# Kernel optimization log

Measured on AMD Instinct MI355X. Metric: run time of the kernel, lower is better.

Reference implementation:

```python
import jax, jax.numpy as jnp
import numpy as np

THRESH_FACTOR = 0.7  # standard TTQ threshold: 0.7 * mean(|W|)

def ternary_quantize(w):
    delta = THRESH_FACTOR * jnp.mean(jnp.abs(w))
    # {-1, 0, +1} ternary weights
    return jnp.where(w > delta, 1.0, jnp.where(w < -delta, -1.0, 0.0)).astype(w.dtype)

def setup_inputs() -> dict:
    key = jax.random.key(0)
    k1, k2, k3 = jax.random.split(key, 3)
    B, S, D_IN, D_OUT = 8, 4096, 1024, 1024
    inp = {
        "input": jax.random.normal(k1, (B, S, D_IN), dtype=jnp.float32),
        "weight": jax.random.normal(k2, (D_OUT, D_IN), dtype=jnp.float32) * (1.0 / np.sqrt(D_IN)),
        "alpha": jnp.ones((1,), dtype=jnp.float32),
        "bias": jax.random.normal(k3, (D_OUT,), dtype=jnp.float32) * (1.0 / np.sqrt(D_IN)),
    }
    return inp

def reference(input, weight, alpha, bias):
    w_ternary = ternary_quantize(weight)          # [out, in] in {-1,0,1}
    w_eff = w_ternary * alpha                     # scalar alpha scale
    # F.linear: y = x @ W^T + b
    out = jnp.einsum('bsd,od->bso', input, w_eff) + bias
    return out
```

## Files before the change

kernel.cpp:

```cpp
#include <hip/hip_runtime.h>
#include <hip/hip_bf16.h>

typedef __bf16 bf16;
typedef __attribute__((ext_vector_type(8))) __bf16 bf16x8;
typedef __attribute__((ext_vector_type(4))) __bf16 bf16x4;
typedef __attribute__((ext_vector_type(4))) float f32x4;

__device__ __forceinline__ void async_load16(const void* g, void* l) {
    __builtin_amdgcn_global_load_lds(
        (const __attribute__((address_space(1))) void*)g,
        (__attribute__((address_space(3))) void*)l, 16, 0, 0);
}

__global__ __launch_bounds__(256) void k_abs_part(const float* __restrict__ w, int n,
                                                  double* __restrict__ part) {
    __shared__ double sd[256];
    const int per_block = n / gridDim.x;
    const int base = blockIdx.x * per_block;
    double s = 0.0;
    for (int i = threadIdx.x; i < per_block; i += 256)
        s += (double)fabsf(w[base + i]);
    sd[threadIdx.x] = s;
    __syncthreads();
    for (int off = 128; off > 0; off >>= 1) {
        if (threadIdx.x < off) sd[threadIdx.x] += sd[threadIdx.x + off];
        __syncthreads();
    }
    if (threadIdx.x == 0) part[blockIdx.x] = sd[0];
}

__global__ __launch_bounds__(256) void k_delta(const double* __restrict__ part, int npart,
                                               int n, float* __restrict__ delta) {
    __shared__ double sd[256];
    double s = 0.0;
    for (int i = threadIdx.x; i < npart; i += 256) s += part[i];
    sd[threadIdx.x] = s;
    __syncthreads();
    for (int off = 128; off > 0; off >>= 1) {
        if (threadIdx.x < off) sd[threadIdx.x] += sd[threadIdx.x + off];
        __syncthreads();
    }
    if (threadIdx.x == 0) *delta = (float)(0.7 * sd[0] / (double)n);
}

__global__ __launch_bounds__(256) void k_quant(const float* __restrict__ w,
                                               const float* __restrict__ dp,
                                               bf16* __restrict__ wt, int n4) {
    const float d = *dp;
    const int i = blockIdx.x * 256 + threadIdx.x;
    if (i >= n4) return;
    const float4 v = ((const float4*)w)[i];
    bf16x4 o;
    o[0] = (bf16)((v.x > d) ? 1.0f : (v.x < -d) ? -1.0f : 0.0f);
    o[1] = (bf16)((v.y > d) ? 1.0f : (v.y < -d) ? -1.0f : 0.0f);
    o[2] = (bf16)((v.z > d) ? 1.0f : (v.z < -d) ? -1.0f : 0.0f);
    o[3] = (bf16)((v.w > d) ? 1.0f : (v.w < -d) ? -1.0f : 0.0f);
    *(bf16x4*)(wt + (size_t)i * 4) = o;
}

__global__ __launch_bounds__(256) void k_gemm(const float* __restrict__ A,
                                              const bf16* __restrict__ Bw,
                                              const float* __restrict__ alphap,
                                              const float* __restrict__ bias,
                                              float* __restrict__ C,
                                              int M, int N, int K) {
    __shared__ bf16 As[128 * 32];
    __shared__ bf16 Bs[128 * 32];

    const int t    = threadIdx.x;
    const int lane = t & 63;
    const int wave = t >> 6;
    const int nbm  = M >> 7;
    const int bm0  = (blockIdx.x % nbm) << 7;
    const int bn0  = (blockIdx.x / nbm) << 7;
    const int wr   = (wave >> 1) << 6;
    const int wc   = (wave & 1) << 6;

    f32x4 acc[4][4] = {};

    const int lr = lane & 15;
    const int lk = (lane >> 4) << 3;

    for (int k0 = 0; k0 < K; k0 += 32) {
        #pragma unroll
        for (int j = 0; j < 2; ++j) {
            const int c = t + j * 256;
            const bf16* src = Bw + (size_t)(bn0 + (c >> 2)) * K + k0 + ((c & 3) << 3);
            async_load16(src, (char*)Bs + j * 4096 + wave * 1024);
        }
        #pragma unroll
        for (int i = 0; i < 4; ++i) {
            const int idx = t + i * 256;
            const int row = idx >> 3;
            const int c4  = (idx & 7) << 2;
            const float4 v = *(const float4*)(A + (size_t)(bm0 + row) * K + k0 + c4);
            bf16x4 h;
            h[0] = (bf16)v.x; h[1] = (bf16)v.y; h[2] = (bf16)v.z; h[3] = (bf16)v.w;
            *(bf16x4*)(As + row * 32 + c4) = h;
        }
        __syncthreads();

        bf16x8 af[4], bfr[4];
        #pragma unroll
        for (int m = 0; m < 4; ++m)
            af[m] = *(const bf16x8*)(As + (wr + m * 16 + lr) * 32 + lk);
        #pragma unroll
        for (int n = 0; n < 4; ++n)
            bfr[n] = *(const bf16x8*)(Bs + (wc + n * 16 + lr) * 32 + lk);
        #pragma unroll
        for (int m = 0; m < 4; ++m)
            #pragma unroll
            for (int n = 0; n < 4; ++n)
                acc[m][n] = __builtin_amdgcn_mfma_f32_16x16x32_bf16(af[m], bfr[n], acc[m][n], 0, 0, 0);
        __syncthreads();
    }

    const float alpha = *alphap;
    float bv[4];
    #pragma unroll
    for (int n = 0; n < 4; ++n) bv[n] = bias[bn0 + wc + n * 16 + lr];

    #pragma unroll
    for (int m = 0; m < 4; ++m) {
        #pragma unroll
        for (int n = 0; n < 4; ++n) {
            const int gcol = bn0 + wc + n * 16 + lr;
            #pragma unroll
            for (int r = 0; r < 4; ++r) {
                const int grow = bm0 + wr + m * 16 + ((lane >> 4) << 2) + r;
                C[(size_t)grow * N + gcol] = alpha * acc[m][n][r] + bv[n];
            }
        }
    }
}

extern "C" void kernel_launch(void* const* d_in, const int* in_sizes, int n_in,
                              void* d_out, int out_size, void* d_ws, size_t ws_size,
                              hipStream_t stream) {
    const float* x     = (const float*)d_in[0];
    const float* w     = (const float*)d_in[1];
    const float* alpha = (const float*)d_in[2];
    const float* bias  = (const float*)d_in[3];
    float* out = (float*)d_out;

    const int wn   = in_sizes[1];
    const int dout = in_sizes[3];
    const int din  = wn / dout;
    const int m    = in_sizes[0] / din;

    char* ws = (char*)d_ws;
    float*  delta = (float*)ws;
    double* part  = (double*)(ws + 64);
    bf16*   wt    = (bf16*)(ws + 8192);

    k_abs_part<<<256, 256, 0, stream>>>(w, wn, part);
    k_delta<<<1, 256, 0, stream>>>(part, 256, wn, delta);
    k_quant<<<(wn / 4 + 255) / 256, 256, 0, stream>>>(w, delta, wt, wn / 4);

    dim3 grid((m / 128) * (dout / 128));
    k_gemm<<<grid, 256, 0, stream>>>(x, wt, alpha, bias, out, m, dout, din);
}
```

Measured before the change: 140.5 us.

## Double-buffer GEMM tiles with BK=64, XOR-swizzled LDS, and XCD-aware block mapping

Rewrites the GEMM main loop to double-buffer the A and B tiles in LDS with a K-tile of 64. The next tile's global loads are issued before the current tile's MFMAs, and the converted A values are written to LDS afterwards, so memory latency overlaps compute and one barrier per iteration is removed. LDS rows are XOR-swizzled in 16-byte slots to avoid bank conflicts, and block IDs are remapped across the 8 XCDs so that N-adjacent tiles sharing A rows land on the same XCD. The cost is doubled LDS (64 KB per block) and more registers for the prefetched floats, with launch_bounds(256,2) set to keep two blocks per CU.

```diff
diff --git a/kernel.cpp b/kernel.cpp
--- a/kernel.cpp
+++ b/kernel.cpp
@@ -58,76 +58,134 @@
     *(bf16x4*)(wt + (size_t)i * 4) = o;
 }
 
-__global__ __launch_bounds__(256) void k_gemm(const float* __restrict__ A,
-                                              const bf16* __restrict__ Bw,
-                                              const float* __restrict__ alphap,
-                                              const float* __restrict__ bias,
-                                              float* __restrict__ C,
-                                              int M, int N, int K) {
-    __shared__ bf16 As[128 * 32];
-    __shared__ bf16 Bs[128 * 32];
+__global__ __launch_bounds__(256, 2) void k_gemm(const float* __restrict__ A,
+                                                 const bf16* __restrict__ Bw,
+                                                 const float* __restrict__ alphap,
+                                                 const float* __restrict__ bias,
+                                                 float* __restrict__ C,
+                                                 int M, int N, int K) {
+    __shared__ __align__(16) bf16 As[2][128 * 64];
+    __shared__ __align__(16) bf16 Bs[2][128 * 64];
 
     const int t    = threadIdx.x;
     const int lane = t & 63;
     const int wave = t >> 6;
-    const int nbm  = M >> 7;
-    const int bm0  = (blockIdx.x % nbm) << 7;
-    const int bn0  = (blockIdx.x / nbm) << 7;
-    const int wr   = (wave >> 1) << 6;
-    const int wc   = (wave & 1) << 6;
+
+    const int nbn = N >> 7;
+    const int cpx = gridDim.x >> 3;
+    const int lid = (blockIdx.x & 7) * cpx + (blockIdx.x >> 3);
+    const int bn0 = (lid & (nbn - 1)) << 7;
+    const int bm0 = (lid / nbn) << 7;
+
+    const int wr = (wave >> 1) << 6;
+    const int wc = (wave & 1) << 6;
+    const int lr = lane & 15;
+    const int hi = lane >> 4;
 
     f32x4 acc[4][4] = {};
 
-    const int lr = lane & 15;
-    const int lk = (lane >> 4) << 3;
-
-    for (int k0 = 0; k0 < K; k0 += 32) {
-        #pragma unroll
-        for (int j = 0; j < 2; ++j) {
-            const int c = t + j * 256;
-            const bf16* src = Bw + (size_t)(bn0 + (c >> 2)) * K + k0 + ((c & 3) << 3);
-            async_load16(src, (char*)Bs + j * 4096 + wave * 1024);
-        }
-        #pragma unroll
-        for (int i = 0; i < 4; ++i) {
-            const int idx = t + i * 256;
-            const int row = idx >> 3;
-            const int c4  = (idx & 7) << 2;
-            const float4 v = *(const float4*)(A + (size_t)(bm0 + row) * K + k0 + c4);
-            bf16x4 h;
-            h[0] = (bf16)v.x; h[1] = (bf16)v.y; h[2] = (bf16)v.z; h[3] = (bf16)v.w;
-            *(bf16x4*)(As + row * 32 + c4) = h;
-        }
-        __syncthreads();
-
-        bf16x8 af[4], bfr[4];
-        #pragma unroll
-        for (int m = 0; m < 4; ++m)
-            af[m] = *(const bf16x8*)(As + (wr + m * 16 + lr) * 32 + lk);
-        #pragma unroll
-        for (int n = 0; n < 4; ++n)
-            bfr[n] = *(const bf16x8*)(Bs + (wc + n * 16 + lr) * 32 + lk);
-        #pragma unroll
-        for (int m = 0; m < 4; ++m)
-            #pragma unroll
-            for (int n = 0; n < 4; ++n)
-                acc[m][n] = __builtin_amdgcn_mfma_f32_16x16x32_bf16(af[m], bfr[n], acc[m][n], 0, 0, 0);
-        __syncthreads();
+    const int a_slot = t & 7;
+    const int a_row0 = t >> 3;
+    const int b_cl   = (wave << 6) | lane;
+    const int b_row0 = b_cl >> 3;
+    const int b_slot = lane & 7;
+
+    const int NT = K >> 6;
+    int cur = 0;
+
+    {
+        #pragma unroll
+        for (int j = 0; j < 4; ++j) {
+            const int row = (j << 5) + b_row0;
+            const int ss  = b_slot ^ (row & 7);
+            async_load16(Bw + (size_t)(bn0 + row) * K + (ss << 3),
+                         (char*)&Bs[0][0] + (j << 12) + (wave << 10));
+        }
+        #pragma unroll
+        for (int u = 0; u < 4; ++u) {
+            const int row = (u << 5) + a_row0;
+            const float4 v0 = *(const float4*)(A + (size_t)(bm0 + row) * K + (a_slot << 3));
+            const float4 v1 = *(const float4*)(A + (size_t)(bm0 + row) * K + (a_slot << 3) + 4);
+            bf16x8 h;
+            h[0] = (bf16)v0.x; h[1] = (bf16)v0.y; h[2] = (bf16)v0.z; h[3] = (bf16)v0.w;
+            h[4] = (bf16)v1.x; h[5] = (bf16)v1.y; h[6] = (bf16)v1.z; h[7] = (bf16)v1.w;
+            *(bf16x8*)((char*)&As[0][0] + row * 128 + ((a_slot ^ (row & 7)) << 4)) = h;
+        }
+        __syncthreads();
+    }
+
+    for (int kt = 0; kt < NT; ++kt) {
+        const int nxt = cur ^ 1;
+        const bool pf = (kt + 1) < NT;
+        const int kn = (kt + 1) << 6;
+        float4 av[8];
+
+        if (pf) {
+            #pragma unroll
+            for (int j = 0; j < 4; ++j) {
+                const int row = (j << 5) + b_row0;
+                const int ss  = b_slot ^ (row & 7);
+                async_load16(Bw + (size_t)(bn0 + row) * K + kn + (ss << 3),
+                             (char*)&Bs[nxt][0] + (j << 12) + (wave << 10));
+            }
+            #pragma unroll
+            for (int u = 0; u < 4; ++u) {
+                const int row = (u << 5) + a_row0;
+                av[2 * u]     = *(const float4*)(A + (size_t)(bm0 + row) * K + kn + (a_slot << 3));
+                av[2 * u + 1] = *(const float4*)(A + (size_t)(bm0 + row) * K + kn + (a_slot << 3) + 4);
+            }
+        }
+
+        #pragma unroll
+        for (int ksub = 0; ksub < 2; ++ksub) {
+            const int ls = (ksub << 2) + hi;
+            bf16x8 af[4], bfm[4];
+            #pragma unroll
+            for (int m = 0; m < 4; ++m) {
+                const int row = wr + (m << 4) + lr;
+                af[m] = *(const bf16x8*)((char*)&As[cur][0] + row * 128 + ((ls ^ (row & 7)) << 4));
+            }
+            #pragma unroll
+            for (int n = 0; n < 4; ++n) {
+                const int row = wc + (n << 4) + lr;
+                bfm[n] = *(const bf16x8*)((char*)&Bs[cur][0] + row * 128 + ((ls ^ (row & 7)) << 4));
+            }
+            #pragma unroll
+            for (int m = 0; m < 4; ++m)
+                #pragma unroll
+                for (int n = 0; n < 4; ++n)
+                    acc[m][n] = __builtin_amdgcn_mfma_f32_16x16x32_bf16(af[m], bfm[n], acc[m][n], 0, 0, 0);
+        }
+
+        if (pf) {
+            #pragma unroll
+            for (int u = 0; u < 4; ++u) {
+                const int row = (u << 5) + a_row0;
+                bf16x8 h;
+                h[0] = (bf16)av[2*u].x;   h[1] = (bf16)av[2*u].y;
+                h[2] = (bf16)av[2*u].z;   h[3] = (bf16)av[2*u].w;
+                h[4] = (bf16)av[2*u+1].x; h[5] = (bf16)av[2*u+1].y;
+                h[6] = (bf16)av[2*u+1].z; h[7] = (bf16)av[2*u+1].w;
+                *(bf16x8*)((char*)&As[nxt][0] + row * 128 + ((a_slot ^ (row & 7)) << 4)) = h;
+            }
+        }
+        __syncthreads();
+        cur = nxt;
     }
 
     const float alpha = *alphap;
     float bv[4];
     #pragma unroll
-    for (int n = 0; n < 4; ++n) bv[n] = bias[bn0 + wc + n * 16 + lr];
+    for (int n = 0; n < 4; ++n) bv[n] = bias[bn0 + wc + (n << 4) + lr];
 
     #pragma unroll
     for (int m = 0; m < 4; ++m) {
         #pragma unroll
         for (int n = 0; n < 4; ++n) {
-            const int gcol = bn0 + wc + n * 16 + lr;
+            const int gcol = bn0 + wc + (n << 4) + lr;
             #pragma unroll
             for (int r = 0; r < 4; ++r) {
-                const int grow = bm0 + wr + m * 16 + ((lane >> 4) << 2) + r;
+                const int grow = bm0 + wr + (m << 4) + (hi << 2) + r;
                 C[(size_t)grow * N + gcol] = alpha * acc[m][n][r] + bv[n];
             }
         }
```

New measurement: 163.9 us. +16.6%, slower.

## Pre-convert activations to bf16 and use 256x256 pipelined GEMM

Applied to the files above, without the earlier changes.

Adds a separate pass that converts the fp32 activations to bf16 in workspace. It then runs a new 512-thread GEMM with 256x256 tiles that double-buffers A and B through async global-to-LDS loads with XOR-swizzled LDS, interleaves loads with MFMA quarter blocks, and uses a grouped block order for L2 reuse. The aim is to remove the per-tile fp32 conversion and the synchronous, non-overlapped loads of the old 128x128 kernel, and to raise data reuse. The cost is an extra full pass over the activations (read fp32, write bf16) and a dependence on workspace size, with the old kernel kept as a fallback.

```diff
diff --git a/kernel.cpp b/kernel.cpp
--- a/kernel.cpp
+++ b/kernel.cpp
@@ -5,6 +5,8 @@
 typedef __attribute__((ext_vector_type(8))) __bf16 bf16x8;
 typedef __attribute__((ext_vector_type(4))) __bf16 bf16x4;
 typedef __attribute__((ext_vector_type(4))) float f32x4;
+
+#define BAR() __builtin_amdgcn_s_barrier()
 
 __device__ __forceinline__ void async_load16(const void* g, void* l) {
     __builtin_amdgcn_global_load_lds(
@@ -58,55 +60,197 @@
     *(bf16x4*)(wt + (size_t)i * 4) = o;
 }
 
-__global__ __launch_bounds__(256) void k_gemm(const float* __restrict__ A,
-                                              const bf16* __restrict__ Bw,
-                                              const float* __restrict__ alphap,
-                                              const float* __restrict__ bias,
-                                              float* __restrict__ C,
-                                              int M, int N, int K) {
+__global__ __launch_bounds__(256) void k_convA(const float* __restrict__ x,
+                                               bf16* __restrict__ y, int n8) {
+    const int stride = gridDim.x * 256;
+    for (int i = blockIdx.x * 256 + threadIdx.x; i < n8; i += stride) {
+        const float4 a = ((const float4*)x)[2 * i];
+        const float4 b = ((const float4*)x)[2 * i + 1];
+        bf16x8 h;
+        h[0] = (bf16)a.x; h[1] = (bf16)a.y; h[2] = (bf16)a.z; h[3] = (bf16)a.w;
+        h[4] = (bf16)b.x; h[5] = (bf16)b.y; h[6] = (bf16)b.z; h[7] = (bf16)b.w;
+        ((bf16x8*)y)[i] = h;
+    }
+}
+
+__device__ __forceinline__ void stage_half(const bf16* __restrict__ srch, int K, int kt,
+                                           char* dst, int t) {
+    #pragma unroll
+    for (int r = 0; r < 2; ++r) {
+        const int c  = (r << 9) + t;
+        const int rp = c >> 3;
+        const int s  = (c & 7) ^ ((t >> 3) & 7);
+        async_load16(srch + (size_t)rp * K + (kt << 6) + (s << 3), dst + (c << 4));
+    }
+}
+
+__global__ __launch_bounds__(512, 2) void k_gemm8(const bf16* __restrict__ A,
+                                                  const bf16* __restrict__ Bw,
+                                                  const float* __restrict__ alphap,
+                                                  const float* __restrict__ bias,
+                                                  float* __restrict__ C,
+                                                  int M, int N, int K) {
+    __shared__ __align__(16) char lds[2][2][2][16384];
+
+    const int t    = threadIdx.x;
+    const int lane = t & 63;
+    const int w    = t >> 6;
+    const int wm   = w >> 2;
+    const int wn   = w & 3;
+    const int lr   = lane & 15;
+    const int hi   = lane >> 4;
+
+    const int nbn = N >> 8;
+    const int cpx = gridDim.x >> 3;
+    const int lid = (blockIdx.x & 7) * cpx + (blockIdx.x >> 3);
+    const int bn0 = (lid % nbn) << 8;
+    const int bm0 = (lid / nbn) << 8;
+
+    const bf16* Asrc[2] = { A  + (size_t)bm0 * K,  A  + (size_t)(bm0 + 128) * K };
+    const bf16* Bsrc[2] = { Bw + (size_t)bn0 * K,  Bw + (size_t)(bn0 + 128) * K };
+
+    f32x4 acc[8][4] = {};
+    bf16x8 afq[4][2], bfA[2][2], bfB[2][2];
+
+    const int x0 = ((hi ^ (lr & 7)) << 4);
+    const int x1 = (((4 + hi) ^ (lr & 7)) << 4);
+
+#define LDA_Q(MQ, PAR) do { \
+    const char* _b = &lds[PAR][0][wm][0]; \
+    _Pragma("unroll") \
+    for (int m = 0; m < 4; ++m) { \
+        const int _r = ((MQ) << 6) + (m << 4) + lr; \
+        afq[m][0] = *(const bf16x8*)(_b + _r * 128 + x0); \
+        afq[m][1] = *(const bf16x8*)(_b + _r * 128 + x1); \
+    } \
+} while (0)
+
+#define LDB_Q(DST, NQ, PAR) do { \
+    const char* _b = &lds[PAR][1][wn >> 1][0]; \
+    _Pragma("unroll") \
+    for (int n = 0; n < 2; ++n) { \
+        const int _r = ((wn & 1) << 6) + ((((NQ) << 1) + n) << 4) + lr; \
+        DST[n][0] = *(const bf16x8*)(_b + _r * 128 + x0); \
+        DST[n][1] = *(const bf16x8*)(_b + _r * 128 + x1); \
+    } \
+} while (0)
+
+#define MF_Q(MQ, NQ, BF) do { \
+    __builtin_amdgcn_s_setprio(1); \
+    _Pragma("unroll") \
+    for (int ks = 0; ks < 2; ++ks) \
+        _Pragma("unroll") \
+        for (int m = 0; m < 4; ++m) { \
+            acc[((MQ)<<2)+m][((NQ)<<1)+0] = __builtin_amdgcn_mfma_f32_16x16x32_bf16(afq[m][ks], BF[0][ks], acc[((MQ)<<2)+m][((NQ)<<1)+0], 0, 0, 0); \
+            acc[((MQ)<<2)+m][((NQ)<<1)+1] = __builtin_amdgcn_mfma_f32_16x16x32_bf16(afq[m][ks], BF[1][ks], acc[((MQ)<<2)+m][((NQ)<<1)+1], 0, 0, 0); \
+        } \
+    __builtin_amdgcn_s_setprio(0); \
+} while (0)
+
+#define VMCNT4() asm volatile("s_waitcnt vmcnt(4)" ::: "memory")
+
+    stage_half(Bsrc[0], K, 0, &lds[0][1][0][0], t);
+    stage_half(Bsrc[1], K, 0, &lds[0][1][1][0], t);
+    stage_half(Asrc[0], K, 0, &lds[0][0][0][0], t);
+    stage_half(Asrc[1], K, 0, &lds[0][0][1][0], t);
+    stage_half(Bsrc[0], K, 1, &lds[1][1][0][0], t);
+    stage_half(Bsrc[1], K, 1, &lds[1][1][1][0], t);
+    asm volatile("s_waitcnt vmcnt(0)" ::: "memory");
+    BAR();
+
+    const int NI = K >> 7;
+    for (int i = 0; i < NI; ++i) {
+        const int  ktB  = 2 * i + 1;
+        const bool last = (i == NI - 1);
+        const int  kA2  = last ? 0 : 2 * i + 2;
+        const int  kB2  = last ? 1 : 2 * i + 3;
+
+        VMCNT4();
+        LDA_Q(0, 0); LDB_Q(bfA, 0, 0);
+        stage_half(Asrc[0], K, ktB, &lds[1][0][0][0], t);
+        BAR(); MF_Q(0, 0, bfA); BAR();
+        LDB_Q(bfB, 1, 0);
+        stage_half(Asrc[1], K, ktB, &lds[1][0][1][0], t);
+        BAR(); MF_Q(0, 1, bfB); BAR();
+        LDA_Q(1, 0);
+        stage_half(Bsrc[0], K, kA2, &lds[0][1][0][0], t);
+        BAR(); MF_Q(1, 1, bfB); BAR();
+        stage_half(Bsrc[1], K, kA2, &lds[0][1][1][0], t);
+        BAR(); MF_Q(1, 0, bfA); BAR();
+
+        VMCNT4();
+        LDA_Q(0, 1); LDB_Q(bfA, 0, 1);
+        stage_half(Asrc[0], K, kA2, &lds[0][0][0][0], t);
+        BAR(); MF_Q(0, 0, bfA); BAR();
+        LDB_Q(bfB, 1, 1);
+        stage_half(Asrc[1], K, kA2, &lds[0][0][1][0], t);
+        BAR(); MF_Q(0, 1, bfB); BAR();
+        LDA_Q(1, 1);
+        stage_half(Bsrc[0], K, kB2, &lds[1][1][0][0], t);
+        BAR(); MF_Q(1, 1, bfB); BAR();
+        stage_half(Bsrc[1], K, kB2, &lds[1][1][1][0], t);
+        BAR(); MF_Q(1, 0, bfA); BAR();
+    }
+
+    const float alpha = *alphap;
+    float bv[4];
+    #pragma unroll
+    for (int nf = 0; nf < 4; ++nf) bv[nf] = bias[bn0 + (wn << 6) + (nf << 4) + lr];
+
+    #pragma unroll
+    for (int mf = 0; mf < 8; ++mf) {
+        const int grow = bm0 + (wm << 7) + (mf << 4) + (hi << 2);
+        #pragma unroll
+        for (int nf = 0; nf < 4; ++nf) {
+            const int gcol = bn0 + (wn << 6) + (nf << 4) + lr;
+            #pragma unroll
+            for (int r = 0; r < 4; ++r)
+                C[(size_t)(grow + r) * N + gcol] = alpha * acc[mf][nf][r] + bv[nf];
+        }
+    }
+#undef LDA_Q
+#undef LDB_Q
+#undef MF_Q
+#undef VMCNT4
+}
+
+__global__ __launch_bounds__(256) void k_gemm_fb(const float* __restrict__ A,
+                                                 const bf16* __restrict__ Bw,
+                                                 const float* __restrict__ alphap,
+                                                 const float* __restrict__ bias,
+                                                 float* __restrict__ C,
+                                                 int M, int N, int K) {
     __shared__ bf16 As[128 * 32];
     __shared__ bf16 Bs[128 * 32];
-
-    const int t    = threadIdx.x;
-    const int lane = t & 63;
-    const int wave = t >> 6;
-    const int nbm  = M >> 7;
-    const int bm0  = (blockIdx.x % nbm) << 7;
-    const int bn0  = (blockIdx.x / nbm) << 7;
-    const int wr   = (wave >> 1) << 6;
-    const int wc   = (wave & 1) << 6;
-
+    const int t = threadIdx.x, lane = t & 63, wave = t >> 6;
+    const int nbm = M >> 7;
+    const int bm0 = (blockIdx.x % nbm) << 7;
+    const int bn0 = (blockIdx.x / nbm) << 7;
+    const int wr = (wave >> 1) << 6, wc = (wave & 1) << 6;
     f32x4 acc[4][4] = {};
-
-    const int lr = lane & 15;
-    const int lk = (lane >> 4) << 3;
-
+    const int lr = lane & 15, lk = (lane >> 4) << 3;
     for (int k0 = 0; k0 < K; k0 += 32) {
         #pragma unroll
         for (int j = 0; j < 2; ++j) {
             const int c = t + j * 256;
-            const bf16* src = Bw + (size_t)(bn0 + (c >> 2)) * K + k0 + ((c & 3) << 3);
-            async_load16(src, (char*)Bs + j * 4096 + wave * 1024);
+            async_load16(Bw + (size_t)(bn0 + (c >> 2)) * K + k0 + ((c & 3) << 3),
+                         (char*)Bs + j * 4096 + wave * 1024);
         }
         #pragma unroll
         for (int i = 0; i < 4; ++i) {
             const int idx = t + i * 256;
-            const int row = idx >> 3;
-            const int c4  = (idx & 7) << 2;
+            const int row = idx >> 3, c4 = (idx & 7) << 2;
             const float4 v = *(const float4*)(A + (size_t)(bm0 + row) * K + k0 + c4);
             bf16x4 h;
             h[0] = (bf16)v.x; h[1] = (bf16)v.y; h[2] = (bf16)v.z; h[3] = (bf16)v.w;
             *(bf16x4*)(As + row * 32 + c4) = h;
         }
         __syncthreads();
-
         bf16x8 af[4], bfr[4];
         #pragma unroll
-        for (int m = 0; m < 4; ++m)
-            af[m] = *(const bf16x8*)(As + (wr + m * 16 + lr) * 32 + lk);
-        #pragma unroll
-        for (int n = 0; n < 4; ++n)
-            bfr[n] = *(const bf16x8*)(Bs + (wc + n * 16 + lr) * 32 + lk);
+        for (int m = 0; m < 4; ++m) af[m] = *(const bf16x8*)(As + (wr + m * 16 + lr) * 32 + lk);
+        #pragma unroll
+        for (int n = 0; n < 4; ++n) bfr[n] = *(const bf16x8*)(Bs + (wc + n * 16 + lr) * 32 + lk);
         #pragma unroll
         for (int m = 0; m < 4; ++m)
             #pragma unroll
@@ -114,31 +258,26 @@
                 acc[m][n] = __builtin_amdgcn_mfma_f32_16x16x32_bf16(af[m], bfr[n], acc[m][n], 0, 0, 0);
         __syncthreads();
     }
-
     const float alpha = *alphap;
-    float bv[4];
     #pragma unroll
-    for (int n = 0; n < 4; ++n) bv[n] = bias[bn0 + wc + n * 16 + lr];
-
-    #pragma unroll
-    for (int m = 0; m < 4; ++m) {
+    for (int m = 0; m < 4; ++m)
         #pragma unroll
         for (int n = 0; n < 4; ++n) {
             const int gcol = bn0 + wc + n * 16 + lr;
+            const float bv = bias[gcol];
             #pragma unroll
             for (int r = 0; r < 4; ++r) {
                 const int grow = bm0 + wr + m * 16 + ((lane >> 4) << 2) + r;
-                C[(size_t)grow * N + gcol] = alpha * acc[m][n][r] + bv[n];
+                C[(size_t)grow * N + gcol] = alpha * acc[m][n][r] + bv;
             }
         }
-    }
 }
 
 extern "C" void kernel_launch(void* const* d_in, const int* in_sizes, int n_in,
                               void* d_out, int out_size, void* d_ws, size_t ws_size,
                               hipStream_t stream) {
     const float* x     = (const float*)d_in[0];
-    const float* w     = (const float*)d_in[1];
+    const float* wgt   = (const float*)d_in[1];
     const float* alpha = (const float*)d_in[2];
     const float* bias  = (const float*)d_in[3];
     float* out = (float*)d_out;
@@ -152,11 +291,19 @@
     float*  delta = (float*)ws;
     double* part  = (double*)(ws + 64);
     bf16*   wt    = (bf16*)(ws + 8192);
-
-    k_abs_part<<<256, 256, 0, stream>>>(w, wn, part);
+    bf16*   abf   = (bf16*)(ws + (4u << 20));
+
+    k_abs_part<<<256, 256, 0, stream>>>(wgt, wn, part);
     k_delta<<<1, 256, 0, stream>>>(part, 256, wn, delta);
-    k_quant<<<(wn / 4 + 255) / 256, 256, 0, stream>>>(w, delta, wt, wn / 4);
-
-    dim3 grid((m / 128) * (dout / 128));
-    k_gemm<<<grid, 256, 0, stream>>>(x, wt, alpha, bias, out, m, dout, din);
-}
+    k_quant<<<(wn / 4 + 255) / 256, 256, 0, stream>>>(wgt, delta, wt, wn / 4);
+
+    const size_t need = (4u << 20) + (size_t)in_sizes[0] * 2;
+    if (ws_size >= need && (m % 256) == 0 && (dout % 256) == 0 && (din % 128) == 0) {
+        k_convA<<<2048, 256, 0, stream>>>(x, abf, in_sizes[0] / 8);
+        dim3 grid((m / 256) * (dout / 256));
+        k_gemm8<<<grid, 512, 0, stream>>>(abf, wt, alpha, bias, out, m, dout, din);
+    } else {
+        dim3 grid((m / 128) * (dout / 128));
+        k_gemm_fb<<<grid, 256, 0, stream>>>(x, wt, alpha, bias, out, m, dout, din);
+    }
+}
```

Result: faster. 128.6 us (-8.5%).
